# Kernel optimization log

Measured on AMD Instinct MI355X. Metric: run time of the kernel, lower is better.

The kernel has to match this reference:

```python
import jax, jax.numpy as jnp
import numpy as np

N_NODES = 100000
N_EDGES = 1600000
D_EDGE = 50
D_NODE = 8


def setup_inputs() -> dict:
    key = jax.random.key(0)
    k1, k2, k3 = jax.random.split(key, 3)
    nodes = jax.random.normal(k1, (N_NODES, D_NODE), dtype=jnp.float32)
    edges = jax.random.normal(k2, (N_EDGES, D_EDGE), dtype=jnp.float32)
    receivers = jax.random.randint(k3, (N_EDGES,), 0, N_NODES, dtype=jnp.int64)
    return {"nodes": nodes, "edges": edges, "receivers": receivers}


def reference(nodes, edges, receivers):
    # torch: zeros(num_nodes, d_edge).index_add(0, receivers, edges)
    num_nodes = nodes.shape[0]
    return jax.ops.segment_sum(edges, receivers, num_segments=num_nodes)
```

## Files before the change

kernel.cpp:

```cpp
#include <hip/hip_runtime.h>


#define N_EDGES   1600000
#define N_GROUPS  (N_EDGES / 4)
#define D_EDGE    50
#define N_NODES   100000

#define NBUCK     4000
#define NPB       25
#define BCAP      768
#define LCAP      120
#define CNT_STRIDE 16

#define BCNT_OFF  0u
#define BIDS_OFF  256000u
#define WS_NEEDED (256000u + 12288000u)

__device__ __forceinline__ int clamp_node(int r) {
    return (r < 0) ? 0 : ((r >= N_NODES) ? N_NODES - 1 : r);
}

__global__ __launch_bounds__(256) void bucket_scatter_kernel(
    const int* __restrict__ receivers, int* __restrict__ bcnt, int* __restrict__ bids)
{
    int idx = blockIdx.x * 256 + threadIdx.x;
    if (idx >= N_GROUPS) return;
    int4 rv = ((const int4*)receivers)[idx];
    int e = idx * 4;
#define SCAT1(comp, k)                                                  \
    {                                                                   \
        int r   = clamp_node(rv.comp);                                  \
        int bkt = r / NPB;                        \
        int lr  = r - bkt * NPB;                                        \
        int p   = atomicAdd(&bcnt[bkt * CNT_STRIDE], 1);                \
        if ((unsigned)p < BCAP) bids[bkt * BCAP + p] = ((e + k) << 5) | lr; \
    }
    SCAT1(x, 0) SCAT1(y, 1) SCAT1(z, 2) SCAT1(w, 3)
#undef SCAT1
}

__global__ __launch_bounds__(256, 8) void bucket_gather_kernel(
    const float* __restrict__ edges, const int* __restrict__ bcnt,
    const int* __restrict__ bids, float* __restrict__ out)
{
    __shared__ int s_list[NPB][LCAP];
    __shared__ int s_lcnt[NPB];

    const int b    = blockIdx.x;
    const int t    = threadIdx.x;
    const int wid  = t >> 6;
    const int lane = t & 63;
    const int l    = (lane < D_EDGE) ? lane : 0;

    if (t < NPB) s_lcnt[t] = 0;
    __syncthreads();

    int cnt = bcnt[b * CNT_STRIDE];
    cnt = (cnt < 0) ? 0 : ((cnt > BCAP) ? BCAP : cnt);

    for (int i = t; i < cnt; i += 256) {
        int v  = bids[b * BCAP + i];
        int e  = v >> 5;
        int lr = v & 31;
        e  = (e < 0 || e >= N_EDGES) ? 0 : e;
        lr = (lr >= NPB) ? NPB - 1 : lr;
        int p = atomicAdd(&s_lcnt[lr], 1);
        if (p < LCAP) s_list[lr][p] = e;
    }
    __syncthreads();

    const int nodeBase = b * NPB;
    for (int ln = wid; ln < NPB; ln += 4) {
        int node = nodeBase + ln;
        if (node >= N_NODES) break;
        int deg = s_lcnt[ln];
        deg = (deg > LCAP) ? LCAP : deg;
        float acc = 0.0f;

#define G16(k) \
        int   e##k = s_list[ln][(j + k < deg) ? (j + k) : 0]; \
        float m##k = (j + k < deg) ? 1.0f : 0.0f; \
        float a##k = edges[e##k * D_EDGE + l];

        for (int j = 0; j < deg; j += 16) {
            G16(0)  G16(1)  G16(2)  G16(3)
            G16(4)  G16(5)  G16(6)  G16(7)
            G16(8)  G16(9)  G16(10) G16(11)
            G16(12) G16(13) G16(14) G16(15)
            acc += (((m0 * a0 + m1 * a1) + (m2 * a2 + m3 * a3))
                  + ((m4 * a4 + m5 * a5) + (m6 * a6 + m7 * a7)))
                 + (((m8 * a8 + m9 * a9) + (m10 * a10 + m11 * a11))
                  + ((m12 * a12 + m13 * a13) + (m14 * a14 + m15 * a15)));
        }
#undef G16

        if (lane < D_EDGE) out[node * D_EDGE + lane] = acc;
    }
}

__global__ __launch_bounds__(256) void scatter_add_kernel(
    const float* __restrict__ edges, const int* __restrict__ receivers,
    float* __restrict__ out)
{
    long long t = (long long)blockIdx.x * blockDim.x + threadIdx.x;
    if (t >= (long long)N_EDGES * D_EDGE) return;
    int e = (int)(t / D_EDGE);
    int d = (int)(t - (long long)e * D_EDGE);
    int r = receivers[e];
    r = clamp_node(r);
    atomicAdd(&out[(long long)r * D_EDGE + d], edges[t]);
}

extern "C" void kernel_launch(void* const* d_in, const int* in_sizes, int n_in,
                              void* d_out, int out_size, void* d_ws, size_t ws_size,
                              hipStream_t stream) {
    const float* edges     = (const float*)d_in[1];
    const int*   receivers = (const int*)d_in[2];
    float*       out       = (float*)d_out;

    if (ws_size < WS_NEEDED || d_ws == nullptr) {
        hipMemsetAsync(d_out, 0, (size_t)out_size * sizeof(float), stream);
        const long long total = (long long)N_EDGES * D_EDGE;
        const int grid = (int)((total + 255) / 256);
        scatter_add_kernel<<<grid, 256, 0, stream>>>(edges, receivers, out);
        return;
    }

    char* ws   = (char*)d_ws;
    int*  bcnt = (int*)(ws + BCNT_OFF);
    int*  bids = (int*)(ws + BIDS_OFF);

    hipMemsetAsync(bcnt, 0, NBUCK * CNT_STRIDE * sizeof(int), stream);

    const int g1 = (N_GROUPS + 255) / 256;
    bucket_scatter_kernel<<<g1, 256, 0, stream>>>(receivers, bcnt, bids);

    bucket_gather_kernel<<<NBUCK, 256, 0, stream>>>(edges, bcnt, bids, out);
}
```

Before: 542.3 us.

## Use coarse buckets with shared-memory binning and sliced gather

Replaces the fine per-25-node global bucketing with 256 coarse buckets of 391 nodes each. Edges are first binned in shared memory per block and flushed to 4 replicated global queues, which cuts global atomic contention. The gather kernel now runs 16 slices per bucket. Each slice scans the whole bucket queue and keeps only its 25 nodes, so bucket lists are read 16 times over. Overflow falls back to per-edge global atomics, and queue capacities could truncate under skewed inputs.

```diff
diff --git a/kernel.cpp b/kernel.cpp
--- a/kernel.cpp
+++ b/kernel.cpp
@@ -6,75 +6,123 @@
 #define D_EDGE    50
 #define N_NODES   100000
 
-#define NBUCK     4000
-#define NPB       25
-#define BCAP      768
-#define LCAP      120
+#define NBUCK     256
+#define NPB_C     391
+#define NREPK     4
+#define QCAP      1920
+#define GPB       512
+#define LCAP1     28
+#define NSLICE    16
+#define SLICE_N   25
+#define LCAP2     120
 #define CNT_STRIDE 16
 
 #define BCNT_OFF  0u
-#define BIDS_OFF  256000u
-#define WS_NEEDED (256000u + 12288000u)
+#define BIDS_OFF  65536u
+#define WS_NEEDED (65536u + 7864320u)
 
 __device__ __forceinline__ int clamp_node(int r) {
     return (r < 0) ? 0 : ((r >= N_NODES) ? N_NODES - 1 : r);
 }
 
-__global__ __launch_bounds__(256) void bucket_scatter_kernel(
+__global__ __launch_bounds__(256, 4) void bucket_scatter_kernel(
     const int* __restrict__ receivers, int* __restrict__ bcnt, int* __restrict__ bids)
 {
-    int idx = blockIdx.x * 256 + threadIdx.x;
-    if (idx >= N_GROUPS) return;
-    int4 rv = ((const int4*)receivers)[idx];
-    int e = idx * 4;
-#define SCAT1(comp, k)                                                  \
-    {                                                                   \
-        int r   = clamp_node(rv.comp);                                  \
-        int bkt = r / NPB;                        \
-        int lr  = r - bkt * NPB;                                        \
-        int p   = atomicAdd(&bcnt[bkt * CNT_STRIDE], 1);                \
-        if ((unsigned)p < BCAP) bids[bkt * BCAP + p] = ((e + k) << 5) | lr; \
+    __shared__ int s_list[NBUCK][LCAP1];
+    __shared__ int s_cnt[NBUCK];
+
+    const int t   = threadIdx.x;
+    const int b   = blockIdx.x;
+    const int rep = b & (NREPK - 1);
+
+    s_cnt[t] = 0;
+    __syncthreads();
+
+    const int gbase = b * GPB;
+    #pragma unroll
+    for (int g = 0; g < GPB / 256; ++g) {
+        int idx = gbase + g * 256 + t;
+        if (idx < N_GROUPS) {
+            int4 rv = ((const int4*)receivers)[idx];
+            int e = idx * 4;
+#define BIN1(comp, k)                                                       \
+            {                                                               \
+                int r   = clamp_node(rv.comp);                              \
+                int bkt = r / NPB_C;                                        \
+                int lr  = r - bkt * NPB_C;                                  \
+                int v   = ((e + k) << 9) | lr;                              \
+                int p   = atomicAdd(&s_cnt[bkt], 1);                        \
+                if (p < LCAP1) {                                            \
+                    s_list[bkt][p] = v;                                     \
+                } else {             \
+                    int q = atomicAdd(&bcnt[(bkt * NREPK + rep) * CNT_STRIDE], 1); \
+                    if ((unsigned)q < QCAP) bids[(bkt * NREPK + rep) * QCAP + q] = v; \
+                }                                                           \
+            }
+            BIN1(x, 0) BIN1(y, 1) BIN1(z, 2) BIN1(w, 3)
+#undef BIN1
+        }
     }
-    SCAT1(x, 0) SCAT1(y, 1) SCAT1(z, 2) SCAT1(w, 3)
-#undef SCAT1
+    __syncthreads();
+
+    int n = s_cnt[t];
+    n = (n > LCAP1) ? LCAP1 : n;
+    if (n > 0) {
+        int base = atomicAdd(&bcnt[(t * NREPK + rep) * CNT_STRIDE], n);
+        int* dst = bids + (t * NREPK + rep) * QCAP;
+        for (int i = 0; i < n; ++i) {
+            int q = base + i;
+            if ((unsigned)q < QCAP) dst[q] = s_list[t][i];
+        }
+    }
 }
 
 __global__ __launch_bounds__(256, 8) void bucket_gather_kernel(
     const float* __restrict__ edges, const int* __restrict__ bcnt,
     const int* __restrict__ bids, float* __restrict__ out)
 {
-    __shared__ int s_list[NPB][LCAP];
-    __shared__ int s_lcnt[NPB];
+    __shared__ int s_list[SLICE_N][LCAP2];
+    __shared__ int s_lcnt[SLICE_N];
 
-    const int b    = blockIdx.x;
+    const int blk  = blockIdx.x;
+    const int bkt  = blk >> 4;
+    const int sl   = blk & (NSLICE - 1);
     const int t    = threadIdx.x;
     const int wid  = t >> 6;
     const int lane = t & 63;
     const int l    = (lane < D_EDGE) ? lane : 0;
 
-    if (t < NPB) s_lcnt[t] = 0;
+    if (t < SLICE_N) s_lcnt[t] = 0;
     __syncthreads();
 
-    int cnt = bcnt[b * CNT_STRIDE];
-    cnt = (cnt < 0) ? 0 : ((cnt > BCAP) ? BCAP : cnt);
+    const int lo = sl * SLICE_N;
+    const int hi = lo + SLICE_N;
 
-    for (int i = t; i < cnt; i += 256) {
-        int v  = bids[b * BCAP + i];
-        int e  = v >> 5;
-        int lr = v & 31;
-        e  = (e < 0 || e >= N_EDGES) ? 0 : e;
-        lr = (lr >= NPB) ? NPB - 1 : lr;
-        int p = atomicAdd(&s_lcnt[lr], 1);
-        if (p < LCAP) s_list[lr][p] = e;
+    #pragma unroll
+    for (int rep = 0; rep < NREPK; ++rep) {
+        int cnt = bcnt[(bkt * NREPK + rep) * CNT_STRIDE];
+        cnt = (cnt < 0) ? 0 : ((cnt > QCAP) ? QCAP : cnt);
+        const int* seg = bids + (bkt * NREPK + rep) * QCAP;
+        for (int i = t; i < cnt; i += 256) {
+            int v  = seg[i];
+            int lr = v & 511;
+            if (lr >= lo && lr < hi) {
+                int e = (int)((unsigned)v >> 9);
+                e = (e >= N_EDGES) ? 0 : e;
+                int p = atomicAdd(&s_lcnt[lr - lo], 1);
+                if (p < LCAP2) s_list[lr - lo][p] = e;
+            }
+        }
     }
     __syncthreads();
 
-    const int nodeBase = b * NPB;
-    for (int ln = wid; ln < NPB; ln += 4) {
-        int node = nodeBase + ln;
-        if (node >= N_NODES) break;
+    for (int ln = wid; ln < SLICE_N; ln += 4) {
+        int lrf = lo + ln;
+        if (lrf >= NPB_C) continue;
+        int node = bkt * NPB_C + lrf;
+        if (node >= N_NODES) continue;
         int deg = s_lcnt[ln];
-        deg = (deg > LCAP) ? LCAP : deg;
+        deg = (deg > LCAP2) ? LCAP2 : deg;
         float acc = 0.0f;
 
 #define G16(k) \
@@ -130,10 +178,10 @@
     int*  bcnt = (int*)(ws + BCNT_OFF);
     int*  bids = (int*)(ws + BIDS_OFF);
 
-    hipMemsetAsync(bcnt, 0, NBUCK * CNT_STRIDE * sizeof(int), stream);
+    hipMemsetAsync(bcnt, 0, NBUCK * NREPK * CNT_STRIDE * sizeof(int), stream);
 
-    const int g1 = (N_GROUPS + 255) / 256;
+    const int g1 = (N_GROUPS + GPB - 1) / GPB;
     bucket_scatter_kernel<<<g1, 256, 0, stream>>>(receivers, bcnt, bids);
 
-    bucket_gather_kernel<<<NBUCK, 256, 0, stream>>>(edges, bcnt, bids, out);
+    bucket_gather_kernel<<<NBUCK * NSLICE, 256, 0, stream>>>(edges, bcnt, bids, out);
 }
```

New measurement: 471.5 us. 1.15x faster.
